# Optimization experiments

Measured on AMD Instinct MI355X. Metric: run time of the kernel, lower is better.

## Reference

```python
import jax, jax.numpy as jnp
import numpy as np

N = 50000
E = 800000
D_IN = 128
D_OUT = 128
LN_EPS = 1e-5
DROP_P = 0.1


def setup_inputs() -> dict:
    key = jax.random.key(0)
    ks = jax.random.split(key, 8)
    x = jax.random.normal(ks[0], (N, D_IN), dtype=jnp.float32)
    edge_index = jax.random.randint(ks[1], (2, E), 0, N, dtype=jnp.int64)
    # dropout mask: binary keep-mask scaled by 1/(1-p), as torch dropout produces
    u = jax.random.uniform(ks[2], (N, D_IN), dtype=jnp.float32)
    dropout_mask = (u > DROP_P).astype(jnp.float32) / (1.0 - DROP_P)
    # LayerNorm affine params
    gamma = jnp.ones((D_IN,), dtype=jnp.float32)
    beta = jnp.zeros((D_IN,), dtype=jnp.float32)
    # SAGEConv linears: lin_l (aggregated neighbors, with bias), lin_r (root, no bias)
    s = 1.0 / np.sqrt(D_IN)
    w_l = jax.random.uniform(ks[3], (D_OUT, D_IN), minval=-s, maxval=s, dtype=jnp.float32)
    b_l = jax.random.uniform(ks[4], (D_OUT,), minval=-s, maxval=s, dtype=jnp.float32)
    w_r = jax.random.uniform(ks[5], (D_OUT, D_IN), minval=-s, maxval=s, dtype=jnp.float32)
    return {"x": x, "edge_index": edge_index, "dropout_mask": dropout_mask,
            "gamma": gamma, "beta": beta, "w_l": w_l, "b_l": b_l, "w_r": w_r}


def reference(x, edge_index, dropout_mask, gamma, beta, w_l, b_l, w_r):
    # LayerNorm + ReLU + dropout mask
    mu = jnp.mean(x, axis=-1, keepdims=True)
    var = jnp.mean(jnp.square(x - mu), axis=-1, keepdims=True)
    h = (x - mu) * jax.lax.rsqrt(var + LN_EPS) * gamma + beta
    h = jax.nn.relu(h) * dropout_mask  # [N, D_IN]
    # SAGEConv: mean-aggregate source features into target nodes
    src = edge_index[0]
    dst = edge_index[1]
    msg = h[src]  # [E, D_IN] gathered messages
    agg = jax.ops.segment_sum(msg, dst, num_segments=N)  # [N, D_IN]
    deg = jax.ops.segment_sum(jnp.ones((E,), dtype=h.dtype), dst, num_segments=N)
    agg = agg / jnp.maximum(deg, 1.0)[:, None]
    # out = lin_l(agg) + lin_r(h)
    out = agg @ w_l.T + b_l + h @ w_r.T  # [N, D_OUT]
    return out
```

## Files before the change

### kernel.cpp

```cpp
#include <hip/hip_runtime.h>
#include <hip/hip_bf16.h>

#define N_NODES 50000
#define N_EDGES 800000
#define D 128
#define NB_SCAN ((N_NODES + 255) / 256)

typedef short bf16x8 __attribute__((ext_vector_type(8)));
typedef float f32x4 __attribute__((ext_vector_type(4)));

__device__ __forceinline__ unsigned int bf16u(float f) {
  __hip_bfloat16 b = __float2bfloat16(f);
  return (unsigned int)*reinterpret_cast<unsigned short*>(&b);
}

__global__ __launch_bounds__(256) void ln_kernel(
    const float* __restrict__ x, const float* __restrict__ mask,
    const float* __restrict__ gamma, const float* __restrict__ beta,
    unsigned int* __restrict__ hb) {
  const int l = threadIdx.x & 63;
  const int n = blockIdx.x * 4 + (threadIdx.x >> 6);
  const float2 xv = ((const float2*)x)[(size_t)n * 64 + l];
  float s = xv.x + xv.y;
  float q = xv.x * xv.x + xv.y * xv.y;
#pragma unroll
  for (int m = 1; m < 64; m <<= 1) {
    s += __shfl_xor(s, m);
    q += __shfl_xor(q, m);
  }
  const float mean = s * (1.0f / 128.0f);
  const float var = q * (1.0f / 128.0f) - mean * mean;
  const float rs = rsqrtf(var + 1e-5f);
  const float2 gv = ((const float2*)gamma)[l];
  const float2 bv = ((const float2*)beta)[l];
  const float2 mv = ((const float2*)mask)[(size_t)n * 64 + l];
  const float h0 = fmaxf((xv.x - mean) * rs * gv.x + bv.x, 0.0f) * mv.x;
  const float h1 = fmaxf((xv.y - mean) * rs * gv.y + bv.y, 0.0f) * mv.y;
  hb[(size_t)n * 64 + l] = (bf16u(h1) << 16) | bf16u(h0);
}

__global__ __launch_bounds__(256) void wt_kernel(
    const float* __restrict__ w_l, const float* __restrict__ w_r,
    unsigned int* __restrict__ wtb) {
  const int i = blockIdx.x * 256 + threadIdx.x;
  const float* src = (i < 8192) ? w_l : w_r;
  const int j = (i < 8192) ? 2 * i : 2 * (i - 8192);
  wtb[i] = (bf16u(src[j + 1]) << 16) | bf16u(src[j]);
}

__global__ __launch_bounds__(256) void gemm_kernel(
    const unsigned short* __restrict__ hb,
    const unsigned short* __restrict__ wtb, const float* __restrict__ b_l,
    unsigned int* __restrict__ gb, float* __restrict__ rp) {
  __shared__ unsigned short Bs[64 * 64 * 8];
  const int t = threadIdx.x;
  const int w = t >> 6;
  const int l = t & 63;
  const int lm = l & 15;
  const int quad = l >> 4;
  const int nb = blockIdx.x * 64;

  int anode = nb + w * 16 + lm;
  if (anode >= N_NODES) anode = N_NODES - 1;
  const unsigned short* arow = hb + (size_t)anode * D + quad * 8;
  bf16x8 af[4];
#pragma unroll
  for (int ch = 0; ch < 4; ++ch) af[ch] = *(const bf16x8*)(arow + ch * 32);

#pragma unroll
  for (int i = 0; i < 16; ++i) {
    const int fid = w * 16 + i;
    const int sub = fid >> 2;
    const int ch = fid & 3;
    const uint4 v = *(const uint4*)(wtb + (size_t)(sub * 16 + lm) * D +
                                    ch * 32 + quad * 8);
    *(uint4*)(Bs + ((size_t)fid * 64 + l) * 8) = v;
  }
  __syncthreads();

  f32x4 acc[16];
#pragma unroll
  for (int sub = 0; sub < 16; ++sub) acc[sub] = (f32x4){0.f, 0.f, 0.f, 0.f};
  const bf16x8* BsF = (const bf16x8*)Bs;
#pragma unroll
  for (int sub = 0; sub < 16; ++sub)
#pragma unroll
    for (int ch = 0; ch < 4; ++ch)
      acc[sub] = __builtin_amdgcn_mfma_f32_16x16x32_bf16(
          af[ch], BsF[(sub * 4 + ch) * 64 + l], acc[sub], 0, 0, 0);

  float blv[8];
#pragma unroll
  for (int j = 0; j < 8; ++j) blv[j] = b_l[j * 16 + lm];

  const int node0 = nb + w * 16 + quad * 4;
#pragma unroll
  for (int reg = 0; reg < 4; ++reg) {
    const int node = node0 + reg;
    if (node < N_NODES) {
      uint4 p;
      p.x = (bf16u(acc[1][reg]) << 16) | bf16u(acc[0][reg]);
      p.y = (bf16u(acc[3][reg]) << 16) | bf16u(acc[2][reg]);
      p.z = (bf16u(acc[5][reg]) << 16) | bf16u(acc[4][reg]);
      p.w = (bf16u(acc[7][reg]) << 16) | bf16u(acc[6][reg]);
      ((uint4*)gb)[(size_t)node * 16 + lm] = p;
      float4 q0, q1;
      q0.x = acc[8][reg] + blv[0];
      q0.y = acc[9][reg] + blv[1];
      q0.z = acc[10][reg] + blv[2];
      q0.w = acc[11][reg] + blv[3];
      q1.x = acc[12][reg] + blv[4];
      q1.y = acc[13][reg] + blv[5];
      q1.z = acc[14][reg] + blv[6];
      q1.w = acc[15][reg] + blv[7];
      ((float4*)rp)[(size_t)node * 32 + lm * 2 + 0] = q0;
      ((float4*)rp)[(size_t)node * 32 + lm * 2 + 1] = q1;
    }
  }
}

__global__ __launch_bounds__(256) void hist_kernel(const int* __restrict__ ei,
                                                   int* __restrict__ deg,
                                                   int* __restrict__ rank) {
  const int e = (blockIdx.x * 256 + threadIdx.x) * 4;
  if (e + 3 < N_EDGES) {
    const int4 d4 = *(const int4*)(ei + N_EDGES + e);
    int4 r4;
    r4.x = atomicAdd(&deg[d4.x], 1);
    r4.y = atomicAdd(&deg[d4.y], 1);
    r4.z = atomicAdd(&deg[d4.z], 1);
    r4.w = atomicAdd(&deg[d4.w], 1);
    *(int4*)(rank + e) = r4;
  } else {
    for (int k = e; k < N_EDGES; ++k)
      rank[k] = atomicAdd(&deg[ei[N_EDGES + k]], 1);
  }
}

__global__ __launch_bounds__(256) void scan1_kernel(
    const int* __restrict__ deg, int* __restrict__ offL1,
    int* __restrict__ partial) {
  __shared__ int sm[256];
  const int t = threadIdx.x;
  const int i = blockIdx.x * 256 + t;
  const int v = (i < N_NODES) ? deg[i] : 0;
  sm[t] = v;
  __syncthreads();
#pragma unroll
  for (int ofs = 1; ofs < 256; ofs <<= 1) {
    int x = sm[t];
    if (t >= ofs) x += sm[t - ofs];
    __syncthreads();
    sm[t] = x;
    __syncthreads();
  }
  if (i < N_NODES) offL1[i] = sm[t] - v;
  if (t == 255) partial[blockIdx.x] = sm[255];
}

__global__ __launch_bounds__(256) void scan2_kernel(int* __restrict__ partial) {
  __shared__ int sm[256];
  const int t = threadIdx.x;
  const int v = (t < NB_SCAN) ? partial[t] : 0;
  sm[t] = v;
  __syncthreads();
#pragma unroll
  for (int ofs = 1; ofs < 256; ofs <<= 1) {
    int x = sm[t];
    if (t >= ofs) x += sm[t - ofs];
    __syncthreads();
    sm[t] = x;
    __syncthreads();
  }
  if (t < NB_SCAN) partial[t] = sm[t] - v;
}

__global__ __launch_bounds__(256) void scatter_kernel(
    const int* __restrict__ ei, const int* __restrict__ offL1,
    const int* __restrict__ partial, const int* __restrict__ rank,
    int* __restrict__ csr) {
  const int e = (blockIdx.x * 256 + threadIdx.x) * 4;
  if (e + 3 < N_EDGES) {
    const int4 s4 = *(const int4*)(ei + e);
    const int4 d4 = *(const int4*)(ei + N_EDGES + e);
    const int4 r4 = *(const int4*)(rank + e);
    csr[offL1[d4.x] + partial[d4.x >> 8] + r4.x] = s4.x;
    csr[offL1[d4.y] + partial[d4.y >> 8] + r4.y] = s4.y;
    csr[offL1[d4.z] + partial[d4.z >> 8] + r4.z] = s4.z;
    csr[offL1[d4.w] + partial[d4.w >> 8] + r4.w] = s4.w;
  } else {
    for (int k = e; k < N_EDGES; ++k) {
      const int dst = ei[N_EDGES + k];
      csr[offL1[dst] + partial[dst >> 8] + rank[k]] = ei[k];
    }
  }
}

#define ACC8(v)                                     \
  do {                                              \
    acc[0] += __uint_as_float((v).x << 16);         \
    acc[1] += __uint_as_float((v).x & 0xffff0000u); \
    acc[2] += __uint_as_float((v).y << 16);         \
    acc[3] += __uint_as_float((v).y & 0xffff0000u); \
    acc[4] += __uint_as_float((v).z << 16);         \
    acc[5] += __uint_as_float((v).z & 0xffff0000u); \
    acc[6] += __uint_as_float((v).w << 16);         \
    acc[7] += __uint_as_float((v).w & 0xffff0000u); \
  } while (0)

__global__ __launch_bounds__(256) void agg_kernel(
    const int* __restrict__ offL1, const int* __restrict__ partial,
    const int* __restrict__ csr, const unsigned int* __restrict__ gb,
    const float* __restrict__ rp, float* __restrict__ out) {
  const int l = threadIdx.x & 63;
  const int q = l >> 4;
  const int c = l & 15;
  const int n = blockIdx.x * 4 + (threadIdx.x >> 6);
  const int s = offL1[n] + partial[n >> 8];
  const int e = (n + 1 < N_NODES) ? offL1[n + 1] + partial[(n + 1) >> 8]
                                  : N_EDGES;
  const uint4* g4 = (const uint4*)gb;
  float acc[8];
#pragma unroll
  for (int k = 0; k < 8; ++k) acc[k] = 0.0f;
  for (int base = s; base < e; base += 64) {
    const int cnt = min(e - base, 64);
    int idx = (l < cnt) ? csr[base + l] : 0;
    int j = 0;
    for (; j + 16 <= cnt; j += 16) {
      const int i0 = __shfl(idx, j + 0 + q);
      const int i1 = __shfl(idx, j + 4 + q);
      const int i2 = __shfl(idx, j + 8 + q);
      const int i3 = __shfl(idx, j + 12 + q);
      const uint4 v0 = g4[(size_t)i0 * 16 + c];
      const uint4 v1 = g4[(size_t)i1 * 16 + c];
      const uint4 v2 = g4[(size_t)i2 * 16 + c];
      const uint4 v3 = g4[(size_t)i3 * 16 + c];
      ACC8(v0);
      ACC8(v1);
      ACC8(v2);
      ACC8(v3);
    }
    for (; j + 4 <= cnt; j += 4) {
      const int i0 = __shfl(idx, j + q);
      const uint4 v0 = g4[(size_t)i0 * 16 + c];
      ACC8(v0);
    }
    if (j < cnt) {
      const int rem = cnt - j;
      const int i0 = __shfl(idx, j + min(q, rem - 1));
      if (q < rem) {
        const uint4 v0 = g4[(size_t)i0 * 16 + c];
        ACC8(v0);
      }
    }
  }
#pragma unroll
  for (int k = 0; k < 8; ++k) {
    acc[k] += __shfl_xor(acc[k], 16);
    acc[k] += __shfl_xor(acc[k], 32);
  }
  if (l < 16) {
    const float inv = 1.0f / fmaxf((float)(e - s), 1.0f);
    const float4 rp0 = ((const float4*)rp)[(size_t)n * 32 + c * 2 + 0];
    const float4 rp1 = ((const float4*)rp)[(size_t)n * 32 + c * 2 + 1];
    float* o = out + (size_t)n * D + c;
    o[0]   = fmaf(acc[0], inv, rp0.x);
    o[16]  = fmaf(acc[1], inv, rp0.y);
    o[32]  = fmaf(acc[2], inv, rp0.z);
    o[48]  = fmaf(acc[3], inv, rp0.w);
    o[64]  = fmaf(acc[4], inv, rp1.x);
    o[80]  = fmaf(acc[5], inv, rp1.y);
    o[96]  = fmaf(acc[6], inv, rp1.z);
    o[112] = fmaf(acc[7], inv, rp1.w);
  }
}

extern "C" void kernel_launch(void* const* d_in, const int* in_sizes, int n_in,
                              void* d_out, int out_size, void* d_ws,
                              size_t ws_size, hipStream_t stream) {
  const float* x = (const float*)d_in[0];
  const int* ei = (const int*)d_in[1];
  const float* mask = (const float*)d_in[2];
  const float* gamma = (const float*)d_in[3];
  const float* beta = (const float*)d_in[4];
  const float* w_l = (const float*)d_in[5];
  const float* b_l = (const float*)d_in[6];
  const float* w_r = (const float*)d_in[7];
  float* out = (float*)d_out;

  char* ws = (char*)d_ws;
  size_t off = 0;
  auto alloc = [&](size_t bytes) {
    char* p = ws + off;
    off += (bytes + 255) & ~(size_t)255;
    return p;
  };
  unsigned int* hb =
      (unsigned int*)alloc((size_t)N_NODES * D * sizeof(unsigned short));
  unsigned int* gb =
      (unsigned int*)alloc((size_t)N_NODES * D * sizeof(unsigned short));
  float* rp = (float*)alloc((size_t)N_NODES * D * sizeof(float));
  unsigned int* wtb =
      (unsigned int*)alloc((size_t)2 * D * D * sizeof(unsigned short));
  int* deg = (int*)alloc((size_t)N_NODES * sizeof(int));
  int* offL1 = (int*)alloc((size_t)N_NODES * sizeof(int));
  int* partial = (int*)alloc((size_t)NB_SCAN * sizeof(int));
  int* rank = (int*)alloc((size_t)N_EDGES * sizeof(int));
  int* csr = (int*)alloc((size_t)N_EDGES * sizeof(int));

  hipMemsetAsync(deg, 0, (size_t)N_NODES * sizeof(int), stream);
  wt_kernel<<<64, 256, 0, stream>>>(w_l, w_r, wtb);
  ln_kernel<<<N_NODES / 4, 256, 0, stream>>>(x, mask, gamma, beta, hb);
  gemm_kernel<<<(N_NODES + 63) / 64, 256, 0, stream>>>(
      (const unsigned short*)hb, (const unsigned short*)wtb, b_l, gb, rp);
  hist_kernel<<<(N_EDGES / 4 + 255) / 256, 256, 0, stream>>>(ei, deg, rank);
  scan1_kernel<<<NB_SCAN, 256, 0, stream>>>(deg, offL1, partial);
  scan2_kernel<<<1, 256, 0, stream>>>(partial);
  scatter_kernel<<<(N_EDGES / 4 + 255) / 256, 256, 0, stream>>>(
      ei, offL1, partial, rank, csr);
  agg_kernel<<<N_NODES / 4, 256, 0, stream>>>(offL1, partial, csr, gb, rp,
                                              out);
}
```

Before: 218.9 us.

## Fuse LayerNorm, weight conversion and degree zeroing into GEMM kernel

```diff
diff --git a/kernel.cpp b/kernel.cpp
--- a/kernel.cpp
+++ b/kernel.cpp
@@ -14,44 +14,12 @@
   return (unsigned int)*reinterpret_cast<unsigned short*>(&b);
 }
 
-__global__ __launch_bounds__(256) void ln_kernel(
+__global__ __launch_bounds__(256) void gemm_kernel(
     const float* __restrict__ x, const float* __restrict__ mask,
     const float* __restrict__ gamma, const float* __restrict__ beta,
-    unsigned int* __restrict__ hb) {
-  const int l = threadIdx.x & 63;
-  const int n = blockIdx.x * 4 + (threadIdx.x >> 6);
-  const float2 xv = ((const float2*)x)[(size_t)n * 64 + l];
-  float s = xv.x + xv.y;
-  float q = xv.x * xv.x + xv.y * xv.y;
-#pragma unroll
-  for (int m = 1; m < 64; m <<= 1) {
-    s += __shfl_xor(s, m);
-    q += __shfl_xor(q, m);
-  }
-  const float mean = s * (1.0f / 128.0f);
-  const float var = q * (1.0f / 128.0f) - mean * mean;
-  const float rs = rsqrtf(var + 1e-5f);
-  const float2 gv = ((const float2*)gamma)[l];
-  const float2 bv = ((const float2*)beta)[l];
-  const float2 mv = ((const float2*)mask)[(size_t)n * 64 + l];
-  const float h0 = fmaxf((xv.x - mean) * rs * gv.x + bv.x, 0.0f) * mv.x;
-  const float h1 = fmaxf((xv.y - mean) * rs * gv.y + bv.y, 0.0f) * mv.y;
-  hb[(size_t)n * 64 + l] = (bf16u(h1) << 16) | bf16u(h0);
-}
-
-__global__ __launch_bounds__(256) void wt_kernel(
     const float* __restrict__ w_l, const float* __restrict__ w_r,
-    unsigned int* __restrict__ wtb) {
-  const int i = blockIdx.x * 256 + threadIdx.x;
-  const float* src = (i < 8192) ? w_l : w_r;
-  const int j = (i < 8192) ? 2 * i : 2 * (i - 8192);
-  wtb[i] = (bf16u(src[j + 1]) << 16) | bf16u(src[j]);
-}
-
-__global__ __launch_bounds__(256) void gemm_kernel(
-    const unsigned short* __restrict__ hb,
-    const unsigned short* __restrict__ wtb, const float* __restrict__ b_l,
-    unsigned int* __restrict__ gb, float* __restrict__ rp) {
+    const float* __restrict__ b_l, unsigned int* __restrict__ gb,
+    float* __restrict__ rp, int* __restrict__ deg) {
   __shared__ unsigned short Bs[64 * 64 * 8];
   const int t = threadIdx.x;
   const int w = t >> 6;
@@ -60,21 +28,73 @@
   const int quad = l >> 4;
   const int nb = blockIdx.x * 64;
 
-  int anode = nb + w * 16 + lm;
-  if (anode >= N_NODES) anode = N_NODES - 1;
-  const unsigned short* arow = hb + (size_t)anode * D + quad * 8;
-  bf16x8 af[4];
-#pragma unroll
-  for (int ch = 0; ch < 4; ++ch) af[ch] = *(const bf16x8*)(arow + ch * 32);
+  if (blockIdx.x < NB_SCAN) {
+    const int i = blockIdx.x * 256 + t;
+    if (i < N_NODES) deg[i] = 0;
+  }
 
 #pragma unroll
   for (int i = 0; i < 16; ++i) {
     const int fid = w * 16 + i;
     const int sub = fid >> 2;
     const int ch = fid & 3;
-    const uint4 v = *(const uint4*)(wtb + (size_t)(sub * 16 + lm) * D +
-                                    ch * 32 + quad * 8);
+    const float* srcw = (sub < 8) ? (w_l + (size_t)(sub * 16 + lm) * D)
+                                  : (w_r + (size_t)((sub - 8) * 16 + lm) * D);
+    const float4 a = *(const float4*)(srcw + ch * 32 + quad * 8);
+    const float4 b = *(const float4*)(srcw + ch * 32 + quad * 8 + 4);
+    uint4 v;
+    v.x = (bf16u(a.y) << 16) | bf16u(a.x);
+    v.y = (bf16u(a.w) << 16) | bf16u(a.z);
+    v.z = (bf16u(b.y) << 16) | bf16u(b.x);
+    v.w = (bf16u(b.w) << 16) | bf16u(b.z);
     *(uint4*)(Bs + ((size_t)fid * 64 + l) * 8) = v;
+  }
+
+  int anode = nb + w * 16 + lm;
+  if (anode >= N_NODES) anode = N_NODES - 1;
+  const float* xrow = x + (size_t)anode * D;
+  float xv[32];
+  float s = 0.f, q = 0.f;
+#pragma unroll
+  for (int ch = 0; ch < 4; ++ch) {
+    const float4 a = *(const float4*)(xrow + ch * 32 + quad * 8);
+    const float4 b = *(const float4*)(xrow + ch * 32 + quad * 8 + 4);
+    xv[ch * 8 + 0] = a.x; xv[ch * 8 + 1] = a.y;
+    xv[ch * 8 + 2] = a.z; xv[ch * 8 + 3] = a.w;
+    xv[ch * 8 + 4] = b.x; xv[ch * 8 + 5] = b.y;
+    xv[ch * 8 + 6] = b.z; xv[ch * 8 + 7] = b.w;
+    s += (a.x + a.y) + (a.z + a.w) + (b.x + b.y) + (b.z + b.w);
+    q += a.x * a.x + a.y * a.y + a.z * a.z + a.w * a.w +
+         b.x * b.x + b.y * b.y + b.z * b.z + b.w * b.w;
+  }
+  s += __shfl_xor(s, 16);
+  s += __shfl_xor(s, 32);
+  q += __shfl_xor(q, 16);
+  q += __shfl_xor(q, 32);
+  const float mean = s * (1.0f / 128.0f);
+  const float var = q * (1.0f / 128.0f) - mean * mean;
+  const float rs = rsqrtf(var + 1e-5f);
+
+  const float* mrow = mask + (size_t)anode * D;
+  bf16x8 af[4];
+#pragma unroll
+  for (int ch = 0; ch < 4; ++ch) {
+    const int c0 = ch * 32 + quad * 8;
+    const float4 g0 = *(const float4*)(gamma + c0);
+    const float4 g1 = *(const float4*)(gamma + c0 + 4);
+    const float4 b0 = *(const float4*)(beta + c0);
+    const float4 b1 = *(const float4*)(beta + c0 + 4);
+    const float4 m0 = *(const float4*)(mrow + c0);
+    const float4 m1 = *(const float4*)(mrow + c0 + 4);
+    const float gv[8] = {g0.x, g0.y, g0.z, g0.w, g1.x, g1.y, g1.z, g1.w};
+    const float bv[8] = {b0.x, b0.y, b0.z, b0.w, b1.x, b1.y, b1.z, b1.w};
+    const float mv[8] = {m0.x, m0.y, m0.z, m0.w, m1.x, m1.y, m1.z, m1.w};
+#pragma unroll
+    for (int j = 0; j < 8; ++j) {
+      const float hv =
+          fmaxf((xv[ch * 8 + j] - mean) * rs * gv[j] + bv[j], 0.0f) * mv[j];
+      af[ch][j] = (short)bf16u(hv);
+    }
   }
   __syncthreads();
 
@@ -296,24 +316,17 @@
     off += (bytes + 255) & ~(size_t)255;
     return p;
   };
-  unsigned int* hb =
-      (unsigned int*)alloc((size_t)N_NODES * D * sizeof(unsigned short));
   unsigned int* gb =
       (unsigned int*)alloc((size_t)N_NODES * D * sizeof(unsigned short));
   float* rp = (float*)alloc((size_t)N_NODES * D * sizeof(float));
-  unsigned int* wtb =
-      (unsigned int*)alloc((size_t)2 * D * D * sizeof(unsigned short));
   int* deg = (int*)alloc((size_t)N_NODES * sizeof(int));
   int* offL1 = (int*)alloc((size_t)N_NODES * sizeof(int));
   int* partial = (int*)alloc((size_t)NB_SCAN * sizeof(int));
   int* rank = (int*)alloc((size_t)N_EDGES * sizeof(int));
   int* csr = (int*)alloc((size_t)N_EDGES * sizeof(int));
 
-  hipMemsetAsync(deg, 0, (size_t)N_NODES * sizeof(int), stream);
-  wt_kernel<<<64, 256, 0, stream>>>(w_l, w_r, wtb);
-  ln_kernel<<<N_NODES / 4, 256, 0, stream>>>(x, mask, gamma, beta, hb);
   gemm_kernel<<<(N_NODES + 63) / 64, 256, 0, stream>>>(
-      (const unsigned short*)hb, (const unsigned short*)wtb, b_l, gb, rp);
+      x, mask, gamma, beta, w_l, w_r, b_l, gb, rp, deg);
   hist_kernel<<<(N_EDGES / 4 + 255) / 256, 256, 0, stream>>>(ei, deg, rank);
   scan1_kernel<<<NB_SCAN, 256, 0, stream>>>(deg, offL1, partial);
   scan2_kernel<<<1, 256, 0, stream>>>(partial);
```

Result: no change. 220.8 us (+0.9%).
